# Kernel tuning notes

Measured on AMD Instinct MI355X. Metric: run time of the kernel, lower is better.

Reference implementation:

```python
import jax, jax.numpy as jnp
import numpy as np

HID, D, NH, NL = 1024, 64, 16, 128  # hidden_dim, head_dim, num_head, num_landmarks


def iterative_inv(mat, n_iter=6):
    # Moore-Penrose pseudo-inverse via Newton-Schulz (Nystromformer), fp32.
    I = jnp.eye(mat.shape[-1], dtype=mat.dtype)
    K = mat
    denom = (jnp.max(jnp.sum(jnp.abs(K), axis=-2), axis=-1)
             * jnp.max(jnp.sum(jnp.abs(K), axis=-1), axis=-1))[..., None, None]
    V = jnp.swapaxes(K, -1, -2) / denom  # Z0 = K^T / (||K||_1 ||K||_inf)
    for _ in range(n_iter):
        KV = K @ V
        V = 0.25 * V @ (13.0 * I - KV @ (15.0 * I - KV @ (7.0 * I - KV)))
    return V


def nystrom_forward(X, mask, Wq, bq, Wk, bk, Wv, bv, Wo, bo):
    B, orig_len, _ = X.shape
    pad_len = NL - orig_len % NL  # always >= 1, matches torch code
    L = orig_len + pad_len
    Xp = jnp.pad(X, ((0, 0), (0, pad_len), (0, 0)))

    def split(Y):  # [B, L, NH*D] -> [B, NH, L, D]
        return Y.reshape(B, L, NH, D).transpose(0, 2, 1, 3)

    Q = split(Xp @ Wq.T + bq).astype(jnp.float32)
    K = split(Xp @ Wk.T + bk).astype(jnp.float32)
    V = split(Xp @ Wv.T + bv).astype(jnp.float32)

    m = mask[:, None, :, None]  # [B,1,L,1]
    scale = 1.0 / (D ** 0.25)   # 1/sqrt(sqrt(head_dim)) applied to both Q and K
    Q = Q * m * scale
    K = K * m * scale

    seg = L // NL
    Q_l = Q.reshape(B, NH, NL, seg, D).mean(axis=-2)  # landmarks via segment means
    K_l = K.reshape(B, NH, NL, seg, D).mean(axis=-2)

    kernel_1 = jax.nn.softmax(jnp.einsum('bhnd,bhld->bhnl', Q, K_l), axis=-1)   # [B,H,L,NL]
    kernel_2 = jax.nn.softmax(jnp.einsum('bhld,bhmd->bhlm', Q_l, K_l), axis=-1)  # [B,H,NL,NL]
    scores_3 = jnp.einsum('bhld,bhnd->bhln', Q_l, K) - 1e9 * (1.0 - mask[:, None, None, :])
    kernel_3 = jax.nn.softmax(scores_3, axis=-1)                                 # [B,H,NL,L]

    out = kernel_1 @ (iterative_inv(kernel_2) @ (kernel_3 @ V))  # [B,H,L,D]
    out = out.transpose(0, 2, 1, 3).reshape(B, L, NH * D)
    out = out @ Wo.T + bo
    return out[:, :orig_len]


def setup_inputs() -> dict:
    key = jax.random.key(0)
    ks = jax.random.split(key, 9)
    B, S = 2, 4095
    Lpad = S + (NL - S % NL)
    s = 0.02
    return {
        'X': jax.random.normal(ks[0], (B, S, HID), dtype=jnp.float32),
        'mask': jnp.ones((B, Lpad), dtype=jnp.float32),
        'Wq': jax.random.normal(ks[1], (NH * D, HID), dtype=jnp.float32) * s,
        'bq': jnp.zeros((NH * D,), dtype=jnp.float32),
        'Wk': jax.random.normal(ks[2], (NH * D, HID), dtype=jnp.float32) * s,
        'bk': jnp.zeros((NH * D,), dtype=jnp.float32),
        'Wv': jax.random.normal(ks[3], (NH * D, HID), dtype=jnp.float32) * s,
        'bv': jnp.zeros((NH * D,), dtype=jnp.float32),
        'Wo': jax.random.normal(ks[4], (HID, NH * D), dtype=jnp.float32) * s,
        'bo': jnp.zeros((HID,), dtype=jnp.float32),
    }


def reference(X, mask, Wq, bq, Wk, bk, Wv, bv, Wo, bo):
    return nystrom_forward(X, mask, Wq, bq, Wk, bk, Wv, bv, Wo, bo)
```

## Files before the change

kernel.cpp:

```cpp
#include <hip/hip_runtime.h>
#include <hip/hip_bf16.h>
#include <math.h>

#define S_ORIG 4095
#define LPAD   4096
#define NHEADS 16
#define DH     64
#define NLM    128
#define BHT    32
#define HIDDEN 1024
#define QKSCALE 0.35355339059327373f

typedef unsigned short u16;
typedef short s16x8 __attribute__((ext_vector_type(8)));
typedef float f32x4 __attribute__((ext_vector_type(4)));

#define IDX64(r, c)  ((r) * 64 + ((c) ^ (((r) & 7) << 3)))
#define IDX128(r, c) ((r) * 128 + ((c) ^ (((r) & 7) << 3)))

__device__ inline void split2(float x, u16& h, u16& l) {
    __hip_bfloat16 bh = __float2bfloat16(x);
    float fh = __bfloat162float(bh);
    __hip_bfloat16 bl = __float2bfloat16(x - fh);
    h = *(u16*)&bh;
    l = *(u16*)&bl;
}

__device__ inline float bf16f(u16 b) {
    unsigned u = ((unsigned)b) << 16;
    return *(float*)&u;
}

__global__ __launch_bounds__(256) void k_split_x(const float* __restrict__ X,
                                                 u16* __restrict__ XH,
                                                 u16* __restrict__ XL) {
    int idx = blockIdx.x * 256 + threadIdx.x;
    int gr = idx >> 8;
    int c4 = (idx & 255) * 4;
    int b = gr >> 12, l = gr & (LPAD - 1);
    float4 v = make_float4(0.f, 0.f, 0.f, 0.f);
    if (l < S_ORIG) v = *(const float4*)(X + ((size_t)b * S_ORIG + l) * HIDDEN + c4);
    ushort4 h4, l4;
    split2(v.x, h4.x, l4.x); split2(v.y, h4.y, l4.y);
    split2(v.z, h4.z, l4.z); split2(v.w, h4.w, l4.w);
    size_t o = (size_t)gr * HIDDEN + c4;
    *(ushort4*)(XH + o) = h4;
    *(ushort4*)(XL + o) = l4;
}

__global__ __launch_bounds__(256) void k_split_w(const float* __restrict__ W,
                                                 u16* __restrict__ WH,
                                                 u16* __restrict__ WL) {
    int idx = blockIdx.x * 256 + threadIdx.x;
    size_t o = (size_t)idx * 4;
    float4 v = *(const float4*)(W + o);
    ushort4 h4, l4;
    split2(v.x, h4.x, l4.x); split2(v.y, h4.y, l4.y);
    split2(v.z, h4.z, l4.z); split2(v.w, h4.w, l4.w);
    *(ushort4*)(WH + o) = h4;
    *(ushort4*)(WL + o) = l4;
}

__global__ __launch_bounds__(256) void k_gemm_bf16(
    const u16* __restrict__ AH, const u16* __restrict__ AL,
    const u16* __restrict__ B0H, const u16* __restrict__ B0L,
    const u16* __restrict__ B1H, const u16* __restrict__ B1L,
    const u16* __restrict__ B2H, const u16* __restrict__ B2L,
    const float* __restrict__ bias0, const float* __restrict__ bias1,
    const float* __restrict__ bias2, const float* __restrict__ mask,
    float* __restrict__ outQ, u16* __restrict__ KPH, u16* __restrict__ KPL,
    u16* __restrict__ VPH, u16* __restrict__ VPL,
    float* __restrict__ outF, int mode)
{
    __shared__ u16 Ah_lds[128 * 64];
    __shared__ u16 Al_lds[128 * 64];
    __shared__ u16 Bh_lds[128 * 64];
    __shared__ u16 Bl_lds[128 * 64];
    int tid = threadIdx.x;
    int seg = (mode == 0) ? (blockIdx.y >> 3) : 0;
    int row0 = blockIdx.x * 128;
    int col0 = (mode == 0) ? ((blockIdx.y & 7) * 128) : (blockIdx.y * 128);
    const u16* BH = (seg == 0) ? B0H : (seg == 1) ? B1H : B2H;
    const u16* BL = (seg == 0) ? B0L : (seg == 1) ? B1L : B2L;
    const float* bias = (seg == 0) ? bias0 : (seg == 1) ? bias1 : bias2;

    int lane = tid & 63, wv = tid >> 6;
    int wr = (wv >> 1) * 64, wc = (wv & 1) * 64;
    int lr = lane & 15, lk = lane >> 4;
    int sr8 = tid >> 3, sc = tid & 7;

    f32x4 acc[4][4] = {};

    for (int kt = 0; kt < 1024; kt += 64) {
        #pragma unroll
        for (int h = 0; h < 4; ++h) {
            int r = sr8 + h * 32;
            int csrc = (sc ^ (r & 7)) * 8;
            size_t ga = (size_t)(row0 + r) * HIDDEN + kt + csrc;
            size_t gb = (size_t)(col0 + r) * HIDDEN + kt + csrc;
            int ldst = r * 64 + sc * 8;
            __builtin_amdgcn_global_load_lds(
                (const __attribute__((address_space(1))) void*)(AH + ga),
                (__attribute__((address_space(3))) void*)(&Ah_lds[ldst]), 16, 0, 0);
            __builtin_amdgcn_global_load_lds(
                (const __attribute__((address_space(1))) void*)(AL + ga),
                (__attribute__((address_space(3))) void*)(&Al_lds[ldst]), 16, 0, 0);
            __builtin_amdgcn_global_load_lds(
                (const __attribute__((address_space(1))) void*)(BH + gb),
                (__attribute__((address_space(3))) void*)(&Bh_lds[ldst]), 16, 0, 0);
            __builtin_amdgcn_global_load_lds(
                (const __attribute__((address_space(1))) void*)(BL + gb),
                (__attribute__((address_space(3))) void*)(&Bl_lds[ldst]), 16, 0, 0);
        }
        __syncthreads();
        #pragma unroll
        for (int kc = 0; kc < 2; ++kc) {
            s16x8 ah[4], al[4], bh4[4], bl4[4];
            #pragma unroll
            for (int i = 0; i < 4; ++i) {
                int ra = wr + i * 16 + lr;
                int rb = wc + i * 16 + lr;
                int ca = (((kc << 2) + lk) ^ (ra & 7)) * 8;
                int cb = (((kc << 2) + lk) ^ (rb & 7)) * 8;
                ah[i]  = *(const s16x8*)&Ah_lds[ra * 64 + ca];
                al[i]  = *(const s16x8*)&Al_lds[ra * 64 + ca];
                bh4[i] = *(const s16x8*)&Bh_lds[rb * 64 + cb];
                bl4[i] = *(const s16x8*)&Bl_lds[rb * 64 + cb];
            }
            #pragma unroll
            for (int i = 0; i < 4; ++i)
                #pragma unroll
                for (int j = 0; j < 4; ++j)
                    acc[i][j] = __builtin_amdgcn_mfma_f32_16x16x32_bf16(ah[i], bh4[j], acc[i][j], 0, 0, 0);
            #pragma unroll
            for (int i = 0; i < 4; ++i)
                #pragma unroll
                for (int j = 0; j < 4; ++j)
                    acc[i][j] = __builtin_amdgcn_mfma_f32_16x16x32_bf16(ah[i], bl4[j], acc[i][j], 0, 0, 0);
            #pragma unroll
            for (int i = 0; i < 4; ++i)
                #pragma unroll
                for (int j = 0; j < 4; ++j)
                    acc[i][j] = __builtin_amdgcn_mfma_f32_16x16x32_bf16(al[i], bh4[j], acc[i][j], 0, 0, 0);
        }
        __syncthreads();
    }

    #pragma unroll
    for (int i = 0; i < 4; ++i) {
        #pragma unroll
        for (int j = 0; j < 4; ++j) {
            int cc = col0 + wc + j * 16 + lr;
            float bval = bias[cc];
            #pragma unroll
            for (int q = 0; q < 4; ++q) {
                int rr = row0 + wr + i * 16 + lk * 4 + q;
                int bb = rr >> 12, l = rr & (LPAD - 1);
                float val = acc[i][j][q] + bval;
                if (mode == 0) {
                    if (seg < 2) val *= mask[(size_t)bb * LPAD + l] * QKSCALE;
                    size_t oi = (((size_t)bb * NHEADS + (cc >> 6)) * LPAD + l) * DH + (cc & 63);
                    if (seg == 0) {
                        outQ[oi] = val;
                    } else {
                        u16 hh2, ll2; split2(val, hh2, ll2);
                        if (seg == 1) { KPH[oi] = hh2; KPL[oi] = ll2; }
                        else          { VPH[oi] = hh2; VPL[oi] = ll2; }
                    }
                } else {
                    if (l < S_ORIG)
                        outF[((size_t)bb * S_ORIG + l) * HIDDEN + cc] = val;
                }
            }
        }
    }
}

__global__ void k_landmarks(const float* __restrict__ Q,
                            const u16* __restrict__ KPH, const u16* __restrict__ KPL,
                            float* __restrict__ QL, float* __restrict__ KL,
                            u16* __restrict__ QLPH, u16* __restrict__ QLPL) {
    int n = blockIdx.x, bh = blockIdx.y, d = threadIdx.x;
    size_t base = ((size_t)bh * LPAD + n * 32) * DH + d;
    float sq = 0.f, sk = 0.f;
    #pragma unroll
    for (int s = 0; s < 32; ++s) {
        sq += Q[base + (size_t)s * DH];
        sk += bf16f(KPH[base + (size_t)s * DH]) + bf16f(KPL[base + (size_t)s * DH]);
    }
    float ql = sq * (1.f / 32.f), kl = sk * (1.f / 32.f);
    size_t oi = ((size_t)bh * NLM + n) * DH + d;
    QL[oi] = ql;
    KL[oi] = kl;
    u16 hh2, ll2; split2(ql, hh2, ll2);
    QLPH[oi] = hh2;
    QLPL[oi] = ll2;
}

__global__ __launch_bounds__(256) void k_qlk(const float* __restrict__ QLb,
                                             const float* __restrict__ Bsrc,
                                             float* __restrict__ out) {
    __shared__ float Qt[64][132];
    __shared__ float Bt[64][132];
    int tid = threadIdx.x;
    int tx = tid & 15, ty = tid >> 4;
    int bh = blockIdx.y;
    const float* QLp = QLb + (size_t)bh * NLM * DH;
    const float* Bp = Bsrc + (size_t)bh * NLM * DH;

    #pragma unroll
    for (int q = 0; q < 8; ++q) {
        int idx = tid + q * 256;
        int r = idx >> 4, d4 = idx & 15;
        float4 v = *(const float4*)(QLp + (size_t)r * DH + d4 * 4);
        Qt[d4 * 4 + 0][r] = v.x; Qt[d4 * 4 + 1][r] = v.y;
        Qt[d4 * 4 + 2][r] = v.z; Qt[d4 * 4 + 3][r] = v.w;
        float4 w = *(const float4*)(Bp + (size_t)r * DH + d4 * 4);
        Bt[d4 * 4 + 0][r] = w.x; Bt[d4 * 4 + 1][r] = w.y;
        Bt[d4 * 4 + 2][r] = w.z; Bt[d4 * 4 + 3][r] = w.w;
    }
    __syncthreads();

    float acc[8][8];
    #pragma unroll
    for (int i = 0; i < 8; ++i)
        #pragma unroll
        for (int j = 0; j < 8; ++j) acc[i][j] = 0.f;

    #pragma unroll
    for (int k = 0; k < 64; ++k) {
        float av[8], bv[8];
        float4 t0 = *(const float4*)&Qt[k][ty * 4];
        float4 t1 = *(const float4*)&Qt[k][64 + ty * 4];
        float4 t2 = *(const float4*)&Bt[k][tx * 4];
        float4 t3 = *(const float4*)&Bt[k][64 + tx * 4];
        av[0]=t0.x; av[1]=t0.y; av[2]=t0.z; av[3]=t0.w;
        av[4]=t1.x; av[5]=t1.y; av[6]=t1.z; av[7]=t1.w;
        bv[0]=t2.x; bv[1]=t2.y; bv[2]=t2.z; bv[3]=t2.w;
        bv[4]=t3.x; bv[5]=t3.y; bv[6]=t3.z; bv[7]=t3.w;
        #pragma unroll
        for (int i = 0; i < 8; ++i)
            #pragma unroll
            for (int j = 0; j < 8; ++j)
                acc[i][j] = fmaf(av[i], bv[j], acc[i][j]);
    }

    float m[8], s[8];
    #pragma unroll
    for (int i = 0; i < 8; ++i) {
        m[i] = acc[i][0];
        #pragma unroll
        for (int j = 1; j < 8; ++j) m[i] = fmaxf(m[i], acc[i][j]);
    }
    #pragma unroll
    for (int o = 8; o >= 1; o >>= 1)
        #pragma unroll
        for (int i = 0; i < 8; ++i) m[i] = fmaxf(m[i], __shfl_xor(m[i], o));
    #pragma unroll
    for (int i = 0; i < 8; ++i) {
        s[i] = 0.f;
        #pragma unroll
        for (int j = 0; j < 8; ++j) {
            acc[i][j] = expf(acc[i][j] - m[i]);
            s[i] += acc[i][j];
        }
    }
    #pragma unroll
    for (int o = 8; o >= 1; o >>= 1)
        #pragma unroll
        for (int i = 0; i < 8; ++i) s[i] += __shfl_xor(s[i], o);
    #pragma unroll
    for (int i = 0; i < 8; ++i) {
        int r = (i >> 2) * 64 + ty * 4 + (i & 3);
        float inv = 1.f / s[i];
        #pragma unroll
        for (int jh = 0; jh < 2; ++jh) {
            int c = jh * 64 + tx * 4;
            float4 res;
            res.x = acc[i][jh * 4 + 0] * inv;
            res.y = acc[i][jh * 4 + 1] * inv;
            res.z = acc[i][jh * 4 + 2] * inv;
            res.w = acc[i][jh * 4 + 3] * inv;
            *(float4*)(out + ((size_t)bh * NLM + r) * NLM + c) = res;
        }
    }
}

__global__ void k_v0denom(const float* __restrict__ K2b, float* __restrict__ V0b) {
    int bh = blockIdx.x, t = threadIdx.x;
    const float* K2 = K2b + (size_t)bh * NLM * NLM;
    float* V0 = V0b + (size_t)bh * NLM * NLM;
    float cs = 0.f, rs = 0.f;
    for (int r = 0; r < NLM; ++r) cs += fabsf(K2[r * NLM + t]);
    for (int c = 0; c < NLM; ++c) rs += fabsf(K2[t * NLM + c]);
    __shared__ float sc[128], sr[128];
    sc[t] = cs; sr[t] = rs;
    __syncthreads();
    for (int s = 64; s > 0; s >>= 1) {
        if (t < s) {
            sc[t] = fmaxf(sc[t], sc[t + s]);
            sr[t] = fmaxf(sr[t], sr[t + s]);
        }
        __syncthreads();
    }
    float invden = 1.f / (sc[0] * sr[0]);
    for (int idx = t; idx < NLM * NLM; idx += 128) {
        int i = idx >> 7, j = idx & 127;
        V0[idx] = K2[j * NLM + i] * invden;
    }
}

__global__ __launch_bounds__(256) void k_bmm(const float* __restrict__ Ab,
                                             const float* __restrict__ Bb,
                                             float* __restrict__ Cb,
                                             float* __restrict__ C2b,
                                             int N, float alpha, float sI,
                                             float alpha2, float sI2) {
    __shared__ float At[128][36];
    __shared__ float Bs[128][36];
    int tid = threadIdx.x;
    int tx = tid & 15, ty = tid >> 4;
    int bh = blockIdx.z;
    int r0 = blockIdx.y * 32, c0 = blockIdx.x * 32;
    const float* A = Ab + (size_t)bh * NLM * NLM;
    const float* Bm = Bb + (size_t)bh * NLM * N;

    #pragma unroll
    for (int q = 0; q < 4; ++q) {
        int idx = tid + q * 256;
        int r = idx >> 5, k4 = idx & 31;
        float4 v = *(const float4*)(A + (size_t)(r0 + r) * NLM + k4 * 4);
        At[k4 * 4 + 0][r] = v.x; At[k4 * 4 + 1][r] = v.y;
        At[k4 * 4 + 2][r] = v.z; At[k4 * 4 + 3][r] = v.w;
        int bk = idx >> 3, c4 = idx & 7;
        float4 w = *(const float4*)(Bm + (size_t)bk * N + c0 + c4 * 4);
        *(float4*)&Bs[bk][c4 * 4] = w;
    }
    __syncthreads();

    float acc[2][2] = {};
    #pragma unroll 8
    for (int k = 0; k < 128; ++k) {
        float2 a2 = *(const float2*)&At[k][ty * 2];
        float2 b2 = *(const float2*)&Bs[k][tx * 2];
        acc[0][0] = fmaf(a2.x, b2.x, acc[0][0]);
        acc[0][1] = fmaf(a2.x, b2.y, acc[0][1]);
        acc[1][0] = fmaf(a2.y, b2.x, acc[1][0]);
        acc[1][1] = fmaf(a2.y, b2.y, acc[1][1]);
    }

    float* C = Cb + (size_t)bh * NLM * N;
    float* C2 = C2b ? (C2b + (size_t)bh * NLM * N) : nullptr;
    #pragma unroll
    for (int i = 0; i < 2; ++i) {
        int gr = r0 + ty * 2 + i;
        #pragma unroll
        for (int j = 0; j < 2; ++j) {
            int gc = c0 + tx * 2 + j;
            float idadd = (gr == gc) ? 1.f : 0.f;
            C[(size_t)gr * N + gc] = alpha * acc[i][j] + sI * idadd;
            if (C2) C2[(size_t)gr * N + gc] = alpha2 * acc[i][j] + sI2 * idadd;
        }
    }
}

__global__ __launch_bounds__(256) void k_flashk3(const u16* __restrict__ QLPH,
                                                 const u16* __restrict__ QLPL,
                                                 const u16* __restrict__ KPH,
                                                 const u16* __restrict__ KPL,
                                                 const u16* __restrict__ VPH,
                                                 const u16* __restrict__ VPL,
                                                 const float* __restrict__ mask,
                                                 float* __restrict__ PO,
                                                 float* __restrict__ ML) {
    __shared__ u16 lds[32768];
    u16* QLh = lds;
    u16* QLl = lds + 4096;
    u16* Kh  = lds + 8192;
    u16* Kl  = lds + 12288;
    u16* Vth = lds + 16384;
    u16* Vtl = lds + 20480;
    u16* Ph  = lds + 24576;
    u16* Pl  = lds + 28672;

    int tid = threadIdx.x;
    int lane = tid & 63, wv = tid >> 6;
    int lr = lane & 15, lk = lane >> 4;
    int sp = blockIdx.x, qh = blockIdx.y, bh = blockIdx.z;
    int b = bh >> 4;
    int q0 = qh * 64;
    int wr16 = wv * 16;

    #pragma unroll
    for (int q = 0; q < 2; ++q) {
        int idx = tid + q * 256;
        int r = idx >> 3, sc = idx & 7;
        int csrc = (sc ^ (r & 7)) * 8;
        size_t g = ((size_t)bh * NLM + q0 + r) * DH + csrc;
        __builtin_amdgcn_global_load_lds(
            (const __attribute__((address_space(1))) void*)(QLPH + g),
            (__attribute__((address_space(3))) void*)(&QLh[idx * 8]), 16, 0, 0);
        __builtin_amdgcn_global_load_lds(
            (const __attribute__((address_space(1))) void*)(QLPL + g),
            (__attribute__((address_space(3))) void*)(&QLl[idx * 8]), 16, 0, 0);
    }

    float m_run[4] = {-1e30f, -1e30f, -1e30f, -1e30f};
    float l_run[4] = {0.f, 0.f, 0.f, 0.f};
    f32x4 t5[4] = {};

    for (int t = 0; t < 8; ++t) {
        int kt0 = sp * 512 + t * 64;
        #pragma unroll
        for (int q = 0; q < 2; ++q) {
            int idx = tid + q * 256;
            int r = idx >> 3, sc = idx & 7;
            int csrc = (sc ^ (r & 7)) * 8;
            size_t g = ((size_t)bh * LPAD + kt0 + r) * DH + csrc;
            __builtin_amdgcn_global_load_lds(
                (const __attribute__((address_space(1))) void*)(KPH + g),
                (__attribute__((address_space(3))) void*)(&Kh[idx * 8]), 16, 0, 0);
            __builtin_amdgcn_global_load_lds(
                (const __attribute__((address_space(1))) void*)(KPL + g),
                (__attribute__((address_space(3))) void*)(&Kl[idx * 8]), 16, 0, 0);
        }
        #pragma unroll
        for (int q = 0; q < 4; ++q) {
            int idx = tid + q * 256;
            int n = idx & 63, dg = idx >> 6;
            int d4 = dg * 4;
            size_t g = ((size_t)bh * LPAD + kt0 + n) * DH + d4;
            ushort4 h4 = *(const ushort4*)(VPH + g);
            ushort4 l4 = *(const ushort4*)(VPL + g);
            #pragma unroll
            for (int e = 0; e < 4; ++e) {
                Vth[IDX64(d4 + e, n)] = (&h4.x)[e];
                Vtl[IDX64(d4 + e, n)] = (&l4.x)[e];
            }
        }
        __syncthreads();

        f32x4 t4[4] = {};
        #pragma unroll
        for (int tt = 0; tt < 3; ++tt) {
            const u16* Xs = (tt == 2) ? QLl : QLh;
            const u16* Ys = (tt == 1) ? Kl : Kh;
            #pragma unroll
            for (int kc = 0; kc < 2; ++kc) {
                s16x8 a = *(const s16x8*)&Xs[IDX64(wr16 + lr, kc * 32 + lk * 8)];
                s16x8 bfr[4];
                #pragma unroll
                for (int j = 0; j < 4; ++j)
                    bfr[j] = *(const s16x8*)&Ys[IDX64(j * 16 + lr, kc * 32 + lk * 8)];
                #pragma unroll
                for (int j = 0; j < 4; ++j)
                    t4[j] = __builtin_amdgcn_mfma_f32_16x16x32_bf16(a, bfr[j], t4[j], 0, 0, 0);
            }
        }

        #pragma unroll
        for (int j = 0; j < 4; ++j) {
            float pen = 1e9f * (1.f - mask[(size_t)b * LPAD + kt0 + j * 16 + lr]);
            #pragma unroll
            for (int q = 0; q < 4; ++q) t4[j][q] -= pen;
        }

        float alpha[4];
        #pragma unroll
        for (int q = 0; q < 4; ++q) {
            float tm = t4[0][q];
            #pragma unroll
            for (int j = 1; j < 4; ++j) tm = fmaxf(tm, t4[j][q]);
            tm = fmaxf(tm, __shfl_xor(tm, 1));
            tm = fmaxf(tm, __shfl_xor(tm, 2));
            tm = fmaxf(tm, __shfl_xor(tm, 4));
            tm = fmaxf(tm, __shfl_xor(tm, 8));
            float mn = fmaxf(m_run[q], tm);
            float al = expf(m_run[q] - mn);
            float s = 0.f;
            #pragma unroll
            for (int j = 0; j < 4; ++j) {
                t4[j][q] = expf(t4[j][q] - mn);
                s += t4[j][q];
            }
            s += __shfl_xor(s, 1);
            s += __shfl_xor(s, 2);
            s += __shfl_xor(s, 4);
            s += __shfl_xor(s, 8);
            l_run[q] = l_run[q] * al + s;
            m_run[q] = mn;
            alpha[q] = al;
        }
        #pragma unroll
        for (int j = 0; j < 4; ++j)
            #pragma unroll
            for (int q = 0; q < 4; ++q) t5[j][q] *= alpha[q];

        #pragma unroll
        for (int j = 0; j < 4; ++j) {
            int col = j * 16 + lr;
            #pragma unroll
            for (int q = 0; q < 4; ++q) {
                int row = wr16 + lk * 4 + q;
                u16 hh2, ll2; split2(t4[j][q], hh2, ll2);
                Ph[IDX64(row, col)] = hh2;
                Pl[IDX64(row, col)] = ll2;
            }
        }
        __syncthreads();

        #pragma unroll
        for (int tt = 0; tt < 3; ++tt) {
            const u16* Xs = (tt == 2) ? Pl : Ph;
            const u16* Ys = (tt == 1) ? Vtl : Vth;
            #pragma unroll
            for (int kc = 0; kc < 2; ++kc) {
                s16x8 a = *(const s16x8*)&Xs[IDX64(wr16 + lr, kc * 32 + lk * 8)];
                s16x8 bfr[4];
                #pragma unroll
                for (int j = 0; j < 4; ++j)
                    bfr[j] = *(const s16x8*)&Ys[IDX64(j * 16 + lr, kc * 32 + lk * 8)];
                #pragma unroll
                for (int j = 0; j < 4; ++j)
                    t5[j] = __builtin_amdgcn_mfma_f32_16x16x32_bf16(a, bfr[j], t5[j], 0, 0, 0);
            }
        }
        __syncthreads();
    }

    size_t pb = (size_t)(bh * 16 + qh * 8 + sp) * 64;
    #pragma unroll
    for (int j = 0; j < 4; ++j) {
        int d = j * 16 + lr;
        #pragma unroll
        for (int q = 0; q < 4; ++q) {
            int row = wr16 + lk * 4 + q;
            PO[(pb + row) * 64 + d] = t5[j][q];
        }
    }
    if (lr == 0) {
        #pragma unroll
        for (int q = 0; q < 4; ++q) {
            int row = wr16 + lk * 4 + q;
            ML[(pb + row) * 2 + 0] = m_run[q];
            ML[(pb + row) * 2 + 1] = l_run[q];
        }
    }
}

__global__ void k_flash_combine(const float* __restrict__ PO,
                                const float* __restrict__ ML,
                                float* __restrict__ K3V) {
    int idx = blockIdx.x * 256 + threadIdx.x;
    int bh = idx >> 13, rem = idx & 8191;
    int g = rem >> 6, d = rem & 63;
    int qh = g >> 6, rl = g & 63;
    size_t rb = (size_t)(bh * 16 + qh * 8) * 64 + rl;
    float mstar = -1e30f;
    #pragma unroll
    for (int sp = 0; sp < 8; ++sp)
        mstar = fmaxf(mstar, ML[(rb + (size_t)sp * 64) * 2]);
    float osum = 0.f, lsum = 0.f;
    #pragma unroll
    for (int sp = 0; sp < 8; ++sp) {
        size_t r = rb + (size_t)sp * 64;
        float wgt = expf(ML[r * 2] - mstar);
        osum += wgt * PO[r * 64 + d];
        lsum += wgt * ML[r * 2 + 1];
    }
    K3V[idx] = osum / lsum;
}

__global__ __launch_bounds__(256) void k_attn(const float* __restrict__ Q,
                                              const float* __restrict__ KLb,
                                              const float* __restrict__ MMb,
                                              u16* __restrict__ ATH,
                                              u16* __restrict__ ATL) {
    __shared__ u16 lds[49152];
    u16* Qh  = lds;
    u16* Ql  = lds + 8192;
    u16* KLh = lds + 16384;
    u16* KLl = lds + 24576;
    u16* Ph  = lds;
    u16* Pl  = lds + 16384;
    u16* Mth = lds + 32768;
    u16* Mtl = lds + 40960;

    int tid = threadIdx.x;
    int lane = tid & 63, wv = tid >> 6;
    int lr = lane & 15, lk = lane >> 4;
    int l0 = blockIdx.x * 128, bh = blockIdx.y;
    int b = bh >> 4, hh = bh & 15;
    int wrA = wv * 32;

    #pragma unroll
    for (int q = 0; q < 4; ++q) {
        int idx = tid + q * 256;
        int r = idx >> 3, c8 = (idx & 7) * 8;
        float4 v0 = *(const float4*)(Q + ((size_t)bh * LPAD + l0 + r) * DH + c8);
        float4 v1 = *(const float4*)(Q + ((size_t)bh * LPAD + l0 + r) * DH + c8 + 4);
        float xs[8] = {v0.x, v0.y, v0.z, v0.w, v1.x, v1.y, v1.z, v1.w};
        s16x8 h8, l8;
        #pragma unroll
        for (int e = 0; e < 8; ++e) {
            u16 hh2, ll2; split2(xs[e], hh2, ll2);
            h8[e] = (short)hh2; l8[e] = (short)ll2;
        }
        *(s16x8*)&Qh[IDX64(r, c8)] = h8;
        *(s16x8*)&Ql[IDX64(r, c8)] = l8;

        float4 w0 = *(const float4*)(KLb + ((size_t)bh * NLM + r) * DH + c8);
        float4 w1 = *(const float4*)(KLb + ((size_t)bh * NLM + r) * DH + c8 + 4);
        float ys[8] = {w0.x, w0.y, w0.z, w0.w, w1.x, w1.y, w1.z, w1.w};
        #pragma unroll
        for (int e = 0; e < 8; ++e) {
            u16 hh2, ll2; split2(ys[e], hh2, ll2);
            h8[e] = (short)hh2; l8[e] = (short)ll2;
        }
        *(s16x8*)&KLh[IDX64(r, c8)] = h8;
        *(s16x8*)&KLl[IDX64(r, c8)] = l8;
    }
    #pragma unroll
    for (int q = 0; q < 8; ++q) {
        int idx = tid + q * 256;
        int n = idx >> 4, d4 = (idx & 15) * 4;
        float4 v = *(const float4*)(MMb + ((size_t)bh * NLM + n) * DH + d4);
        float xs[4] = {v.x, v.y, v.z, v.w};
        #pragma unroll
        for (int e = 0; e < 4; ++e) {
            u16 hh2, ll2; split2(xs[e], hh2, ll2);
            Mth[IDX128(d4 + e, n)] = hh2;
            Mtl[IDX128(d4 + e, n)] = ll2;
        }
    }
    __syncthreads();

    f32x4 t4[2][8] = {};
    #pragma unroll
    for (int t = 0; t < 3; ++t) {
        const u16* Xs = (t == 2) ? Ql : Qh;
        const u16* Ys = (t == 1) ? KLl : KLh;
        #pragma unroll
        for (int kc = 0; kc < 2; ++kc) {
            s16x8 a[2], bfr[8];
            #pragma unroll
            for (int i = 0; i < 2; ++i)
                a[i] = *(const s16x8*)&Xs[IDX64(wrA + i * 16 + lr, kc * 32 + lk * 8)];
            #pragma unroll
            for (int j = 0; j < 8; ++j)
                bfr[j] = *(const s16x8*)&Ys[IDX64(j * 16 + lr, kc * 32 + lk * 8)];
            #pragma unroll
            for (int i = 0; i < 2; ++i)
                #pragma unroll
                for (int j = 0; j < 8; ++j)
                    t4[i][j] = __builtin_amdgcn_mfma_f32_16x16x32_bf16(a[i], bfr[j], t4[i][j], 0, 0, 0);
        }
    }

    #pragma unroll
    for (int i = 0; i < 2; ++i)
        #pragma unroll
        for (int q = 0; q < 4; ++q) {
            float m = t4[i][0][q];
            #pragma unroll
            for (int j = 1; j < 8; ++j) m = fmaxf(m, t4[i][j][q]);
            m = fmaxf(m, __shfl_xor(m, 1));
            m = fmaxf(m, __shfl_xor(m, 2));
            m = fmaxf(m, __shfl_xor(m, 4));
            m = fmaxf(m, __shfl_xor(m, 8));
            float s = 0.f;
            #pragma unroll
            for (int j = 0; j < 8; ++j) {
                t4[i][j][q] = expf(t4[i][j][q] - m);
                s += t4[i][j][q];
            }
            s += __shfl_xor(s, 1);
            s += __shfl_xor(s, 2);
            s += __shfl_xor(s, 4);
            s += __shfl_xor(s, 8);
            float inv = 1.f / s;
            #pragma unroll
            for (int j = 0; j < 8; ++j) t4[i][j][q] *= inv;
        }

    __syncthreads();
    #pragma unroll
    for (int i = 0; i < 2; ++i)
        #pragma unroll
        for (int j = 0; j < 8; ++j) {
            int col = j * 16 + lr;
            #pragma unroll
            for (int q = 0; q < 4; ++q) {
                int row = wrA + i * 16 + lk * 4 + q;
                u16 hh2, ll2; split2(t4[i][j][q], hh2, ll2);
                Ph[IDX128(row, col)] = hh2;
                Pl[IDX128(row, col)] = ll2;
            }
        }
    __syncthreads();

    f32x4 t5[2][4] = {};
    #pragma unroll
    for (int t = 0; t < 3; ++t) {
        const u16* Xs = (t == 2) ? Pl : Ph;
        const u16* Ys = (t == 1) ? Mtl : Mth;
        #pragma unroll
        for (int kc = 0; kc < 4; ++kc) {
            s16x8 a[2], bfr[4];
            #pragma unroll
            for (int i = 0; i < 2; ++i)
                a[i] = *(const s16x8*)&Xs[IDX128(wrA + i * 16 + lr, kc * 32 + lk * 8)];
            #pragma unroll
            for (int j = 0; j < 4; ++j)
                bfr[j] = *(const s16x8*)&Ys[IDX128(j * 16 + lr, kc * 32 + lk * 8)];
            #pragma unroll
            for (int i = 0; i < 2; ++i)
                #pragma unroll
                for (int j = 0; j < 4; ++j)
                    t5[i][j] = __builtin_amdgcn_mfma_f32_16x16x32_bf16(a[i], bfr[j], t5[i][j], 0, 0, 0);
        }
    }

    #pragma unroll
    for (int i = 0; i < 2; ++i)
        #pragma unroll
        for (int j = 0; j < 4; ++j) {
            int d = j * 16 + lr;
            #pragma unroll
            for (int q = 0; q < 4; ++q) {
                int l = l0 + wrA + i * 16 + lk * 4 + q;
                size_t base = ((size_t)b * LPAD + l) * HIDDEN + hh * DH + d;
                u16 hh2, ll2; split2(t5[i][j][q], hh2, ll2);
                ATH[base] = hh2;
                ATL[base] = ll2;
            }
        }
}

extern "C" void kernel_launch(void* const* d_in, const int* in_sizes, int n_in,
                              void* d_out, int out_size, void* d_ws, size_t ws_size,
                              hipStream_t stream) {
    (void)in_sizes; (void)n_in; (void)out_size; (void)ws_size;
    const float* X    = (const float*)d_in[0];
    const float* mask = (const float*)d_in[1];
    const float* Wq   = (const float*)d_in[2];
    const float* bq   = (const float*)d_in[3];
    const float* Wk   = (const float*)d_in[4];
    const float* bk   = (const float*)d_in[5];
    const float* Wv   = (const float*)d_in[6];
    const float* bv   = (const float*)d_in[7];
    const float* Wo   = (const float*)d_in[8];
    const float* bo   = (const float*)d_in[9];
    float* out = (float*)d_out;
    float* w = (float*)d_ws;

    size_t o = 0;
    u16* WQH = (u16*)(w + o); o += (size_t)HIDDEN * HIDDEN / 2;
    u16* WQL = (u16*)(w + o); o += (size_t)HIDDEN * HIDDEN / 2;
    u16* WKH = (u16*)(w + o); o += (size_t)HIDDEN * HIDDEN / 2;
    u16* WKL = (u16*)(w + o); o += (size_t)HIDDEN * HIDDEN / 2;
    u16* WVH = (u16*)(w + o); o += (size_t)HIDDEN * HIDDEN / 2;
    u16* WVL = (u16*)(w + o); o += (size_t)HIDDEN * HIDDEN / 2;
    u16* WOH = (u16*)(w + o); o += (size_t)HIDDEN * HIDDEN / 2;
    u16* WOL = (u16*)(w + o); o += (size_t)HIDDEN * HIDDEN / 2;
    float* Q   = w + o; o += (size_t)BHT * LPAD * DH;
    float* K   = w + o; o += (size_t)BHT * LPAD * DH;
    float* V   = w + o; o += (size_t)BHT * LPAD * DH;
    float* QL  = w + o; o += (size_t)BHT * NLM * DH;
    float* KL  = w + o; o += (size_t)BHT * NLM * DH;
    float* K2  = w + o; o += (size_t)BHT * NLM * NLM;
    float* VA  = w + o; o += (size_t)BHT * NLM * NLM;
    float* VB  = w + o; o += (size_t)BHT * NLM * NLM;
    float* KV  = w + o; o += (size_t)BHT * NLM * NLM;
    float* P1  = w + o; o += (size_t)BHT * NLM * NLM;
    float* T3  = w + o; o += (size_t)BHT * NLM * NLM;
    float* PK  = w + o; o += (size_t)BHT * 16 * NLM * DH;
    float* K3V = w + o; o += (size_t)BHT * NLM * DH;
    float* MM  = w + o; o += (size_t)BHT * NLM * DH;
    float* SC  = w + o; o += (size_t)BHT * NLM * LPAD;

    u16* KPH = (u16*)K;
    u16* KPL = KPH + (size_t)BHT * LPAD * DH;
    u16* VPH = (u16*)V;
    u16* VPL = VPH + (size_t)BHT * LPAD * DH;

    float* PO = PK;
    float* ML = PK + (size_t)BHT * 16 * 64 * 64;

    u16* XH  = (u16*)SC;
    u16* XL  = XH + (size_t)2 * LPAD * HIDDEN;
    u16* ATH = (u16*)SC;
    u16* ATL = ATH + (size_t)2 * LPAD * HIDDEN;
    u16* QLPH = (u16*)SC + (size_t)32 * 1024 * 1024;
    u16* QLPL = QLPH + (size_t)BHT * NLM * DH;

    k_split_x<<<8192, 256, 0, stream>>>(X, XH, XL);
    k_split_w<<<1024, 256, 0, stream>>>(Wq, WQH, WQL);
    k_split_w<<<1024, 256, 0, stream>>>(Wk, WKH, WKL);
    k_split_w<<<1024, 256, 0, stream>>>(Wv, WVH, WVL);
    k_split_w<<<1024, 256, 0, stream>>>(Wo, WOH, WOL);

    k_gemm_bf16<<<dim3(64, 24), 256, 0, stream>>>(
        XH, XL, WQH, WQL, WKH, WKL, WVH, WVL, bq, bk, bv, mask,
        Q, KPH, KPL, VPH, VPL, nullptr, 0);

    k_landmarks<<<dim3(NLM, BHT), 64, 0, stream>>>(Q, KPH, KPL, QL, KL, QLPH, QLPL);

    k_qlk<<<dim3(1, BHT), 256, 0, stream>>>(QL, KL, K2);

    k_flashk3<<<dim3(8, 2, BHT), 256, 0, stream>>>(QLPH, QLPL, KPH, KPL, VPH, VPL, mask, PO, ML);
    k_flash_combine<<<(BHT * NLM * DH) / 256, 256, 0, stream>>>(PO, ML, K3V);

    k_v0denom<<<BHT, 128, 0, stream>>>(K2, VA);
    float* cur = VA;
    float* nxt = VB;
    for (int it = 0; it < 6; ++it) {
        k_bmm<<<dim3(4, 4, BHT), 256, 0, stream>>>(K2, cur, KV, P1, NLM, 1.f, 0.f, -1.f, 7.f);
        k_bmm<<<dim3(4, 4, BHT), 256, 0, stream>>>(KV, P1, T3, nullptr, NLM, -1.f, 15.f, 0.f, 0.f);
        k_bmm<<<dim3(4, 4, BHT), 256, 0, stream>>>(KV, T3, P1, nullptr, NLM, -1.f, 13.f, 0.f, 0.f);
        k_bmm<<<dim3(4, 4, BHT), 256, 0, stream>>>(cur, P1, nxt, nullptr, NLM, 0.25f, 0.f, 0.f, 0.f);
        float* t = cur; cur = nxt; nxt = t;
    }

    k_bmm<<<dim3(2, 4, BHT), 256, 0, stream>>>(cur, K3V, MM, nullptr, DH, 1.f, 0.f, 0.f, 0.f);

    k_attn<<<dim3(32, BHT), 256, 0, stream>>>(Q, KL, MM, ATH, ATL);

    k_gemm_bf16<<<dim3(64, 8), 256, 0, stream>>>(
        ATH, ATL, WOH, WOL, nullptr, nullptr, nullptr, nullptr, bo, nullptr,
        nullptr, nullptr, nullptr, nullptr, nullptr, nullptr, nullptr, out, 1);
}
```

Measured before the change: 568.8 us.

## Store Q as bf16 hi/lo pairs, fuse v0 denom into qlk, merge weight splits

The QKV GEMM now writes Q as split bf16 high/low pairs, like K and V. This lets k_attn load Q straight into LDS with global_load_lds instead of re-splitting fp32 values, and k_landmarks reads the pairs. The Newton-Schulz initial V0 (norm-based denominator plus transpose) is computed inside the qlk softmax kernel, which removes a separate kernel and a reread of K2. The four weight-split launches are merged into one 2D launch. One __syncthreads in the flash kernel is also removed, which saves a barrier but could introduce an LDS race.

```diff
diff --git a/kernel.cpp b/kernel.cpp
--- a/kernel.cpp
+++ b/kernel.cpp
@@ -48,17 +48,25 @@
     *(ushort4*)(XL + o) = l4;
 }
 
-__global__ __launch_bounds__(256) void k_split_w(const float* __restrict__ W,
-                                                 u16* __restrict__ WH,
-                                                 u16* __restrict__ WL) {
+__global__ __launch_bounds__(256) void k_split_w4(
+    const float* __restrict__ W0, const float* __restrict__ W1,
+    const float* __restrict__ W2, const float* __restrict__ W3,
+    u16* __restrict__ H0, u16* __restrict__ L0,
+    u16* __restrict__ H1, u16* __restrict__ L1,
+    u16* __restrict__ H2, u16* __restrict__ L2,
+    u16* __restrict__ H3, u16* __restrict__ L3) {
+    int ws = blockIdx.y;
+    const float* W = (ws == 0) ? W0 : (ws == 1) ? W1 : (ws == 2) ? W2 : W3;
+    u16* H = (ws == 0) ? H0 : (ws == 1) ? H1 : (ws == 2) ? H2 : H3;
+    u16* L = (ws == 0) ? L0 : (ws == 1) ? L1 : (ws == 2) ? L2 : L3;
     int idx = blockIdx.x * 256 + threadIdx.x;
     size_t o = (size_t)idx * 4;
     float4 v = *(const float4*)(W + o);
     ushort4 h4, l4;
     split2(v.x, h4.x, l4.x); split2(v.y, h4.y, l4.y);
     split2(v.z, h4.z, l4.z); split2(v.w, h4.w, l4.w);
-    *(ushort4*)(WH + o) = h4;
-    *(ushort4*)(WL + o) = l4;
+    *(ushort4*)(H + o) = h4;
+    *(ushort4*)(L + o) = l4;
 }
 
 __global__ __launch_bounds__(256) void k_gemm_bf16(
@@ -68,7 +76,8 @@
     const u16* __restrict__ B2H, const u16* __restrict__ B2L,
     const float* __restrict__ bias0, const float* __restrict__ bias1,
     const float* __restrict__ bias2, const float* __restrict__ mask,
-    float* __restrict__ outQ, u16* __restrict__ KPH, u16* __restrict__ KPL,
+    u16* __restrict__ QPH, u16* __restrict__ QPL,
+    u16* __restrict__ KPH, u16* __restrict__ KPL,
     u16* __restrict__ VPH, u16* __restrict__ VPL,
     float* __restrict__ outF, int mode)
 {
@@ -83,6 +92,8 @@
     const u16* BH = (seg == 0) ? B0H : (seg == 1) ? B1H : B2H;
     const u16* BL = (seg == 0) ? B0L : (seg == 1) ? B1L : B2L;
     const float* bias = (seg == 0) ? bias0 : (seg == 1) ? bias1 : bias2;
+    u16* PH = (seg == 0) ? QPH : (seg == 1) ? KPH : VPH;
+    u16* PL = (seg == 0) ? QPL : (seg == 1) ? KPL : VPL;
 
     int lane = tid & 63, wv = tid >> 6;
     int wr = (wv >> 1) * 64, wc = (wv & 1) * 64;
@@ -160,13 +171,9 @@
                 if (mode == 0) {
                     if (seg < 2) val *= mask[(size_t)bb * LPAD + l] * QKSCALE;
                     size_t oi = (((size_t)bb * NHEADS + (cc >> 6)) * LPAD + l) * DH + (cc & 63);
-                    if (seg == 0) {
-                        outQ[oi] = val;
-                    } else {
-                        u16 hh2, ll2; split2(val, hh2, ll2);
-                        if (seg == 1) { KPH[oi] = hh2; KPL[oi] = ll2; }
-                        else          { VPH[oi] = hh2; VPL[oi] = ll2; }
-                    }
+                    u16 hh2, ll2; split2(val, hh2, ll2);
+                    PH[oi] = hh2;
+                    PL[oi] = ll2;
                 } else {
                     if (l < S_ORIG)
                         outF[((size_t)bb * S_ORIG + l) * HIDDEN + cc] = val;
@@ -176,7 +183,7 @@
     }
 }
 
-__global__ void k_landmarks(const float* __restrict__ Q,
+__global__ void k_landmarks(const u16* __restrict__ QPH, const u16* __restrict__ QPL,
                             const u16* __restrict__ KPH, const u16* __restrict__ KPL,
                             float* __restrict__ QL, float* __restrict__ KL,
                             u16* __restrict__ QLPH, u16* __restrict__ QLPL) {
@@ -185,8 +192,9 @@
     float sq = 0.f, sk = 0.f;
     #pragma unroll
     for (int s = 0; s < 32; ++s) {
-        sq += Q[base + (size_t)s * DH];
-        sk += bf16f(KPH[base + (size_t)s * DH]) + bf16f(KPL[base + (size_t)s * DH]);
+        size_t a = base + (size_t)s * DH;
+        sq += bf16f(QPH[a]) + bf16f(QPL[a]);
+        sk += bf16f(KPH[a]) + bf16f(KPL[a]);
     }
     float ql = sq * (1.f / 32.f), kl = sk * (1.f / 32.f);
     size_t oi = ((size_t)bh * NLM + n) * DH + d;
@@ -197,11 +205,13 @@
     QLPL[oi] = ll2;
 }
 
-__global__ __launch_bounds__(256) void k_qlk(const float* __restrict__ QLb,
-                                             const float* __restrict__ Bsrc,
-                                             float* __restrict__ out) {
+__global__ __launch_bounds__(256) void k_qlk_v0(const float* __restrict__ QLb,
+                                                const float* __restrict__ Bsrc,
+                                                float* __restrict__ K2out,
+                                                float* __restrict__ VA) {
     __shared__ float Qt[64][132];
     __shared__ float Bt[64][132];
+    __shared__ float redx[256];
     int tid = threadIdx.x;
     int tx = tid & 15, ty = tid >> 4;
     int bh = blockIdx.y;
@@ -271,42 +281,77 @@
         for (int i = 0; i < 8; ++i) s[i] += __shfl_xor(s[i], o);
     #pragma unroll
     for (int i = 0; i < 8; ++i) {
+        float inv = 1.f / s[i];
+        #pragma unroll
+        for (int j = 0; j < 8; ++j) acc[i][j] *= inv;
+    }
+
+    #pragma unroll
+    for (int i = 0; i < 8; ++i) {
         int r = (i >> 2) * 64 + ty * 4 + (i & 3);
-        float inv = 1.f / s[i];
         #pragma unroll
         for (int jh = 0; jh < 2; ++jh) {
             int c = jh * 64 + tx * 4;
             float4 res;
-            res.x = acc[i][jh * 4 + 0] * inv;
-            res.y = acc[i][jh * 4 + 1] * inv;
-            res.z = acc[i][jh * 4 + 2] * inv;
-            res.w = acc[i][jh * 4 + 3] * inv;
-            *(float4*)(out + ((size_t)bh * NLM + r) * NLM + c) = res;
-        }
-    }
-}
-
-__global__ void k_v0denom(const float* __restrict__ K2b, float* __restrict__ V0b) {
-    int bh = blockIdx.x, t = threadIdx.x;
-    const float* K2 = K2b + (size_t)bh * NLM * NLM;
-    float* V0 = V0b + (size_t)bh * NLM * NLM;
-    float cs = 0.f, rs = 0.f;
-    for (int r = 0; r < NLM; ++r) cs += fabsf(K2[r * NLM + t]);
-    for (int c = 0; c < NLM; ++c) rs += fabsf(K2[t * NLM + c]);
-    __shared__ float sc[128], sr[128];
-    sc[t] = cs; sr[t] = rs;
+            res.x = acc[i][jh * 4 + 0]; res.y = acc[i][jh * 4 + 1];
+            res.z = acc[i][jh * 4 + 2]; res.w = acc[i][jh * 4 + 3];
+            *(float4*)(K2out + ((size_t)bh * NLM + r) * NLM + c) = res;
+        }
+    }
+
+    float rmax = 0.f;
+    #pragma unroll
+    for (int i = 0; i < 8; ++i) {
+        float rs = 0.f;
+        #pragma unroll
+        for (int j = 0; j < 8; ++j) rs += acc[i][j];
+        rs += __shfl_xor(rs, 1);
+        rs += __shfl_xor(rs, 2);
+        rs += __shfl_xor(rs, 4);
+        rs += __shfl_xor(rs, 8);
+        rmax = fmaxf(rmax, rs);
+    }
+    redx[tid] = rmax;
     __syncthreads();
-    for (int s = 64; s > 0; s >>= 1) {
-        if (t < s) {
-            sc[t] = fmaxf(sc[t], sc[t + s]);
-            sr[t] = fmaxf(sr[t], sr[t + s]);
-        }
+    for (int st = 128; st > 0; st >>= 1) {
+        if (tid < st) redx[tid] = fmaxf(redx[tid], redx[tid + st]);
         __syncthreads();
     }
-    float invden = 1.f / (sc[0] * sr[0]);
-    for (int idx = t; idx < NLM * NLM; idx += 128) {
-        int i = idx >> 7, j = idx & 127;
-        V0[idx] = K2[j * NLM + i] * invden;
+    float rmax_blk = redx[0];
+    __syncthreads();
+
+    float* colbuf = &Qt[0][0];
+    #pragma unroll
+    for (int j = 0; j < 8; ++j) {
+        int c = (j >> 2) * 64 + tx * 4 + (j & 3);
+        float cp = 0.f;
+        #pragma unroll
+        for (int i = 0; i < 8; ++i) cp += acc[i][j];
+        colbuf[ty * 128 + c] = cp;
+    }
+    __syncthreads();
+    float cs = 0.f;
+    if (tid < 128) {
+        #pragma unroll
+        for (int t2 = 0; t2 < 16; ++t2) cs += colbuf[t2 * 128 + tid];
+    }
+    redx[tid] = cs;
+    __syncthreads();
+    for (int st = 128; st > 0; st >>= 1) {
+        if (tid < st) redx[tid] = fmaxf(redx[tid], redx[tid + st]);
+        __syncthreads();
+    }
+    float invden = 1.f / (rmax_blk * redx[0]);
+
+    float* VAp = VA + (size_t)bh * NLM * NLM;
+    #pragma unroll
+    for (int i = 0; i < 8; ++i) {
+        int r = (i >> 2) * 64 + ty * 4 + (i & 3);
+        #pragma unroll
+        for (int j = 0; j < 8; ++j) {
+            int c = (j >> 2) * 64 + tx * 4 + (j & 3);
+            VAp[(size_t)c * NLM + r] = acc[i][j] * invden;
+        }
     }
 }
 
@@ -507,7 +552,6 @@
                 Pl[IDX64(row, col)] = ll2;
             }
         }
-        __syncthreads();
 
         #pragma unroll
         for (int tt = 0; tt < 3; ++tt) {
@@ -571,7 +615,8 @@
     K3V[idx] = osum / lsum;
 }
 
-__global__ __launch_bounds__(256) void k_attn(const float* __restrict__ Q,
+__global__ __launch_bounds__(256) void k_attn(const u16* __restrict__ QPH,
+                                              const u16* __restrict__ QPL,
                                               const float* __restrict__ KLb,
                                               const float* __restrict__ MMb,
                                               u16* __restrict__ ATH,
@@ -596,22 +641,24 @@
     #pragma unroll
     for (int q = 0; q < 4; ++q) {
         int idx = tid + q * 256;
+        int r = idx >> 3, sc = idx & 7;
+        int csrc = (sc ^ (r & 7)) * 8;
+        size_t g = ((size_t)bh * LPAD + l0 + r) * DH + csrc;
+        __builtin_amdgcn_global_load_lds(
+            (const __attribute__((address_space(1))) void*)(QPH + g),
+            (__attribute__((address_space(3))) void*)(&Qh[idx * 8]), 16, 0, 0);
+        __builtin_amdgcn_global_load_lds(
+            (const __attribute__((address_space(1))) void*)(QPL + g),
+            (__attribute__((address_space(3))) void*)(&Ql[idx * 8]), 16, 0, 0);
+    }
+    #pragma unroll
+    for (int q = 0; q < 4; ++q) {
+        int idx = tid + q * 256;
         int r = idx >> 3, c8 = (idx & 7) * 8;
-        float4 v0 = *(const float4*)(Q + ((size_t)bh * LPAD + l0 + r) * DH + c8);
-        float4 v1 = *(const float4*)(Q + ((size_t)bh * LPAD + l0 + r) * DH + c8 + 4);
-        float xs[8] = {v0.x, v0.y, v0.z, v0.w, v1.x, v1.y, v1.z, v1.w};
-        s16x8 h8, l8;
-        #pragma unroll
-        for (int e = 0; e < 8; ++e) {
-            u16 hh2, ll2; split2(xs[e], hh2, ll2);
-            h8[e] = (short)hh2; l8[e] = (short)ll2;
-        }
-        *(s16x8*)&Qh[IDX64(r, c8)] = h8;
-        *(s16x8*)&Ql[IDX64(r, c8)] = l8;
-
         float4 w0 = *(const float4*)(KLb + ((size_t)bh * NLM + r) * DH + c8);
         float4 w1 = *(const float4*)(KLb + ((size_t)bh * NLM + r) * DH + c8 + 4);
         float ys[8] = {w0.x, w0.y, w0.z, w0.w, w1.x, w1.y, w1.z, w1.w};
+        s16x8 h8, l8;
         #pragma unroll
         for (int e = 0; e < 8; ++e) {
             u16 hh2, ll2; split2(ys[e], hh2, ll2);
@@ -779,6 +826,8 @@
     float* MM  = w + o; o += (size_t)BHT * NLM * DH;
     float* SC  = w + o; o += (size_t)BHT * NLM * LPAD;
 
+    u16* QPH = (u16*)Q;
+    u16* QPL = QPH + (size_t)BHT * LPAD * DH;
     u16* KPH = (u16*)K;
     u16* KPL = KPH + (size_t)BHT * LPAD * DH;
     u16* VPH = (u16*)V;
@@ -795,23 +844,20 @@
     u16* QLPL = QLPH + (size_t)BHT * NLM * DH;
 
     k_split_x<<<8192, 256, 0, stream>>>(X, XH, XL);
-    k_split_w<<<1024, 256, 0, stream>>>(Wq, WQH, WQL);
-    k_split_w<<<1024, 256, 0, stream>>>(Wk, WKH, WKL);
-    k_split_w<<<1024, 256, 0, stream>>>(Wv, WVH, WVL);
-    k_split_w<<<1024, 256, 0, stream>>>(Wo, WOH, WOL);
+    k_split_w4<<<dim3(1024, 4), 256, 0, stream>>>(Wq, Wk, Wv, Wo,
+        WQH, WQL, WKH, WKL, WVH, WVL, WOH, WOL);
 
     k_gemm_bf16<<<dim3(64, 24), 256, 0, stream>>>(
         XH, XL, WQH, WQL, WKH, WKL, WVH, WVL, bq, bk, bv, mask,
-        Q, KPH, KPL, VPH, VPL, nullptr, 0);
-
-    k_landmarks<<<dim3(NLM, BHT), 64, 0, stream>>>(Q, KPH, KPL, QL, KL, QLPH, QLPL);
-
-    k_qlk<<<dim3(1, BHT), 256, 0, stream>>>(QL, KL, K2);
+        QPH, QPL, KPH, KPL, VPH, VPL, nullptr, 0);
+
+    k_landmarks<<<dim3(NLM, BHT), 64, 0, stream>>>(QPH, QPL, KPH, KPL, QL, KL, QLPH, QLPL);
+
+    k_qlk_v0<<<dim3(1, BHT), 256, 0, stream>>>(QL, KL, K2, VA);
 
     k_flashk3<<<dim3(8, 2, BHT), 256, 0, stream>>>(QLPH, QLPL, KPH, KPL, VPH, VPL, mask, PO, ML);
     k_flash_combine<<<(BHT * NLM * DH) / 256, 256, 0, stream>>>(PO, ML, K3V);
 
-    k_v0denom<<<BHT, 128, 0, stream>>>(K2, VA);
     float* cur = VA;
     float* nxt = VB;
     for (int it = 0; it < 6; ++it) {
@@ -824,9 +870,9 @@
 
     k_bmm<<<dim3(2, 4, BHT), 256, 0, stream>>>(cur, K3V, MM, nullptr, DH, 1.f, 0.f, 0.f, 0.f);
 
-    k_attn<<<dim3(32, BHT), 256, 0, stream>>>(Q, KL, MM, ATH, ATL);
+    k_attn<<<dim3(32, BHT), 256, 0, stream>>>(QPH, QPL, KL, MM, ATH, ATL);
 
     k_gemm_bf16<<<dim3(64, 8), 256, 0, stream>>>(
         ATH, ATL, WOH, WOL, nullptr, nullptr, nullptr, nullptr, bo, nullptr,
-        nullptr, nullptr, nullptr, nullptr, nullptr, nullptr, nullptr, out, 1);
-}
+        nullptr, nullptr, nullptr, nullptr, nullptr, nullptr, nullptr, nullptr, out, 1);
+}
```

Measured after the change: 541.1 us (median of 3 runs). 1.05x faster.
